# Performance work log

Measured on AMD Instinct MI355X. Metric: run time of the kernel, lower is better.

## Reference

```python
import jax, jax.numpy as jnp
import numpy as np

RRELU_SLOPE = (1.0 / 8.0 + 1.0 / 3.0) / 2.0  # F.rrelu eval-mode slope
DILATIONS = (1, 2, 4, 8)
HIDDEN_TEMP = 1.0
GUMBEL_TEMP = 0.1


def rrelu(x):
    return jnp.where(x >= 0, x, RRELU_SLOPE * x)


def conv1d(x, w, b, dilation):
    # x: [B, Cin, T], w: [Cout, Cin, K] -> [B, Cout, T'] (VALID, dilated)
    y = jax.lax.conv_general_dilated(
        x, w, window_strides=(1,), padding='VALID', rhs_dilation=(dilation,),
        dimension_numbers=('NCH', 'OIH', 'NCH'))
    return y + b[None, :, None]


def setup_inputs() -> dict:
    key = jax.random.key(0)
    ks = jax.random.split(key, 16)
    B, D, T, R = 8, 32, 4096, 8
    s = 0.05  # param scale for numerical stability
    inp = {
        'x': jax.random.normal(ks[0], (B, D, T), jnp.float32),
        'u': jax.random.uniform(ks[1], (B, T, R), jnp.float32, 1e-6, 1.0 - 1e-6),
        'conv_w0': jax.random.normal(ks[2], (128, D, 2), jnp.float32) * s,
        'conv_b0': jax.random.normal(ks[3], (128,), jnp.float32) * s,
        'conv_w1': jax.random.normal(ks[4], (128, 128, 2), jnp.float32) * s,
        'conv_b1': jax.random.normal(ks[5], (128,), jnp.float32) * s,
        'conv_w2': jax.random.normal(ks[6], (128, 128, 2), jnp.float32) * s,
        'conv_b2': jax.random.normal(ks[7], (128,), jnp.float32) * s,
        'conv_w3': jax.random.normal(ks[8], (R, 128, 2), jnp.float32) * s,
        'conv_b3': jax.random.normal(ks[9], (R,), jnp.float32) * s,
        'pw0': jax.random.normal(ks[10], (R, 256, 128), jnp.float32) * s,
        'pb0': jax.random.normal(ks[11], (R, 256), jnp.float32) * s,
        'pw1': jax.random.normal(ks[12], (R, 2 * D, 256), jnp.float32) * s,
        'pb1': jax.random.normal(ks[13], (R, 2 * D), jnp.float32) * s,
    }
    return inp


def reference(x, u, conv_w0, conv_b0, conv_w1, conv_b1, conv_w2, conv_b2,
              conv_w3, conv_b3, pw0, pb0, pw1, pb1):
    pad = sum(DILATIONS)  # causal left pad
    h = jnp.pad(x, ((0, 0), (0, 0), (pad, 0)))
    for w, b, d in ((conv_w0, conv_b0, DILATIONS[0]),
                    (conv_w1, conv_b1, DILATIONS[1]),
                    (conv_w2, conv_b2, DILATIONS[2])):
        h = rrelu(conv1d(h, w, b, d))
    pre = h  # [B, 128, T + dilations[-1]]
    h_vecs = rrelu(conv1d(pre, conv_w3, conv_b3, DILATIONS[3]))  # [B, R, T]
    pre = pre[:, :, DILATIONS[3]:]  # [B, 128, T]

    p = jax.nn.softmax(h_vecs / HIDDEN_TEMP, axis=1)  # [B, R, T]
    logits = jnp.log(p).transpose(0, 2, 1)  # [B, T, R]
    g = -jnp.log(-jnp.log(u))  # gumbel noise from uniform input
    gen_z = jax.nn.softmax((logits + g) / GUMBEL_TEMP, axis=-1).transpose(0, 2, 1)  # [B, R, T]

    # Fused mixture-of-experts dynamic linear: equal to materializing
    # einsum('brt,roi->boit') then contracting with pre, but avoids the huge tensor.
    params = (jnp.einsum('brt,roi,bit->bot', gen_z, pw0, pre)
              + jnp.einsum('brt,ro->bot', gen_z, pb0))
    # NOTE: original calls F.rrelu(params) without assignment -> no-op (kept faithful)
    params = (jnp.einsum('brt,roi,bit->bot', gen_z, pw1, params)
              + jnp.einsum('brt,ro->bot', gen_z, pb1))

    mus, sig = jnp.split(params, 2, axis=1)  # each [B, n_dims, T]
    sigmas = 0.5 + 0.5 * jnp.tanh(sig) + 0.001
    return mus, sigmas, gen_z
```

## Files before the change

### kernel.cpp

```cpp
#include <hip/hip_runtime.h>
#include <math.h>

typedef __attribute__((ext_vector_type(8))) short bf16x8;
typedef __attribute__((ext_vector_type(4))) float f32x4;
struct __align__(8)  us4 { unsigned short x,y,z,w; };
struct __align__(16) ui4 { unsigned x,y,z,w; };

#define SLOPE 0.2291666666666667f
constexpr int N0=4110, N1=4108, N2=4104, NX=4111;

__device__ __forceinline__ unsigned short f2bf(float f){
  unsigned u = __float_as_uint(f);
  u = (u + 0x7FFF + ((u>>16)&1)) >> 16;
  return (unsigned short)u;
}
__device__ __forceinline__ float bf2f(unsigned short h){
  return __uint_as_float(((unsigned)h)<<16);
}
__device__ __forceinline__ float rrelu(float v){ return v>=0.f ? v : v*SLOPE; }

__global__ __launch_bounds__(256) void prep_w(
  const float* __restrict__ w0, const float* __restrict__ w1, const float* __restrict__ w2,
  const float* __restrict__ pw0, const float* __restrict__ pw1,
  const float* __restrict__ pb0, const float* __restrict__ pb1,
  unsigned short* __restrict__ w0e, unsigned short* __restrict__ w1e, unsigned short* __restrict__ w2e,
  unsigned short* __restrict__ pw0b, unsigned short* __restrict__ pw1b,
  unsigned short* __restrict__ pb0e, unsigned short* __restrict__ pb1e)
{
  int idx = blockIdx.x*256 + threadIdx.x;
  if (idx < 8192){ int oc=idx>>6, k=idx&63, tap=k>>5, i=k&31;
    w0e[idx] = f2bf(w0[(oc*32+i)*2+tap]); return; }
  idx -= 8192;
  if (idx < 32768){ int oc=idx>>8, k=idx&255, tap=k>>7, i=k&127;
    w1e[idx] = f2bf(w1[(oc*128+i)*2+tap]); return; }
  idx -= 32768;
  if (idx < 32768){ int oc=idx>>8, k=idx&255, tap=k>>7, i=k&127;
    w2e[idx] = f2bf(w2[(oc*128+i)*2+tap]); return; }
  idx -= 32768;
  if (idx < 262144){ pw0b[idx] = f2bf(pw0[idx]); return; }
  idx -= 262144;
  if (idx < 131072){ pw1b[idx] = f2bf(pw1[idx]); return; }
  idx -= 131072;
  if (idx < 8192){ int o=idx>>5, r=idx&31; pb0e[idx] = r<8 ? f2bf(pb0[r*256+o]) : (unsigned short)0; return; }
  idx -= 8192;
  if (idx < 2048){ int o=idx>>5, r=idx&31; pb1e[idx] = r<8 ? f2bf(pb1[r*64+o]) : (unsigned short)0; return; }
}

__global__ __launch_bounds__(64) void prep_xt(const float* __restrict__ x,
                                              unsigned short* __restrict__ xt)
{
  __shared__ float s[32][64];
  const int b = blockIdx.y, j0 = blockIdx.x*64, l = threadIdx.x;
  #pragma unroll 4
  for (int i=0;i<32;i++){
    int p = j0 + l - 15;
    s[i][l] = (p>=0 && p<4096) ? x[((size_t)b*32+i)*4096+p] : 0.f;
  }
  __syncthreads();
  const int j = j0 + l;
  if (j < NX){
    unsigned tmp[16];
    #pragma unroll
    for (int q=0;q<16;q++)
      tmp[q] = (unsigned)f2bf(s[2*q][l]) | ((unsigned)f2bf(s[2*q+1][l])<<16);
    ui4* dst = (ui4*)(xt + ((size_t)b*NX + j)*32);
    #pragma unroll
    for (int q=0;q<4;q++){ ui4 v={tmp[4*q],tmp[4*q+1],tmp[4*q+2],tmp[4*q+3]}; dst[q]=v; }
  }
}

template<int IC, int DIL, int NIN, int NOUT>
__global__ __launch_bounds__(256) void conv_g(
    const unsigned short* __restrict__ act,
    const unsigned short* __restrict__ wgt,
    const float* __restrict__ bias,
    unsigned short* __restrict__ outp)
{
  constexpr int KT   = 2*IC;
  constexpr int NK   = KT/32;
  constexpr int NH   = (KT > 128) ? 2 : 1;
  constexpr int KPH  = KT / NH;
  constexpr int NKH  = KPH/32;
  constexpr int HRB  = KPH*2;
  constexpr int HCPR = HRB/16;
  __shared__ __align__(16) char wsm[64*HRB];
  __shared__ __align__(16) char outs[64*128];

  const int tid = threadIdx.x;
  const int b = blockIdx.z, ob = blockIdx.y, tb = blockIdx.x*64;
  const int o0g = ob*64;
  const int wid = tid>>6, l = tid&63, lo = l&15, hi = l>>4;

  bf16x8 bfr[NK];
  {
    const int tg = tb + wid*16 + lo;
    const int te = tg < NOUT ? tg : NOUT-1;
    #pragma unroll
    for (int kk=0;kk<NK;kk++){
      int k = kk*32 + hi*8;
      int tap = (k >= IC) ? 1 : 0;
      int off = k - tap*IC;
      bfr[kk] = *(const bf16x8*)(act + ((size_t)b*NIN + te + tap*DIL)*IC + off);
    }
  }

  f32x4 acc[4];
  #pragma unroll
  for (int m=0;m<4;m++) acc[m] = (f32x4){0.f,0.f,0.f,0.f};

  #pragma unroll
  for (int h=0; h<NH; ++h){
    __syncthreads();
    for (int c = tid; c < 64*HCPR; c += 256){
      int row = c / HCPR, cc = c % HCPR;
      ui4 v = *(const ui4*)((const char*)wgt + (size_t)(o0g+row)*KT*2 + h*HRB + cc*16);
      *(ui4*)(wsm + row*HRB + ((cc*16) ^ ((row&7)<<4))) = v;
    }
    __syncthreads();
    #pragma unroll
    for (int kk=0;kk<NKH;kk++){
      #pragma unroll
      for (int m=0;m<4;m++){
        int row = m*16 + lo;
        bf16x8 af = *(const bf16x8*)(wsm + row*HRB + ((kk*64+hi*16) ^ ((row&7)<<4)));
        acc[m] = __builtin_amdgcn_mfma_f32_16x16x32_bf16(af, bfr[h*NKH+kk], acc[m], 0,0,0);
      }
    }
  }
  __syncthreads();
  #pragma unroll
  for (int m=0;m<4;m++){
    const int ol = m*16 + hi*4;
    float b0v = bias[o0g+ol+0], b1v = bias[o0g+ol+1], b2v = bias[o0g+ol+2], b3v = bias[o0g+ol+3];
    int tl = wid*16 + lo;
    us4 v;
    v.x = f2bf(rrelu(acc[m][0] + b0v));
    v.y = f2bf(rrelu(acc[m][1] + b1v));
    v.z = f2bf(rrelu(acc[m][2] + b2v));
    v.w = f2bf(rrelu(acc[m][3] + b3v));
    *(us4*)(outs + tl*128 + ((ol*2) ^ ((tl&7)<<4))) = v;
  }
  __syncthreads();
  #pragma unroll
  for (int i=0;i<2;i++){
    int c = tid + i*256;
    int row = c>>3, cc = c&7;
    if (tb + row < NOUT){
      ui4 v = *(const ui4*)(outs + row*128 + ((cc*16) ^ ((row&7)<<4)));
      *(ui4*)(outp + ((size_t)b*NOUT + tb + row)*128 + o0g + cc*8) = v;
    }
  }
}

__global__ __launch_bounds__(64) void gumbel_g(
  const unsigned short* __restrict__ h2t,
  const float* __restrict__ w3, const float* __restrict__ b3,
  const float* __restrict__ u,
  float* __restrict__ genz,
  unsigned short* __restrict__ zt)
{
  __shared__ unsigned hs[72][66];
  const int b = blockIdx.y, t0 = blockIdx.x*64, l = threadIdx.x;
  const unsigned* src = (const unsigned*)(h2t + ((size_t)b*N2 + t0)*128);
  for (int e=l; e<72*64; e+=64) hs[e>>6][e&63] = src[e];
  __syncthreads();

  float acc[8];
  #pragma unroll
  for (int r=0;r<8;r++) acc[r]=b3[r];
  for (int i2=0;i2<64;i2++){
    unsigned a0 = hs[l][i2], a1 = hs[l+8][i2];
    float v00 = bf2f(a0&0xffff), v01 = bf2f(a0>>16);
    float v10 = bf2f(a1&0xffff), v11 = bf2f(a1>>16);
    const int i = 2*i2;
    #pragma unroll
    for (int r=0;r<8;r++){
      acc[r] = fmaf(w3[(r*128+i)*2],     v00, acc[r]);
      acc[r] = fmaf(w3[(r*128+i)*2+1],   v10, acc[r]);
      acc[r] = fmaf(w3[(r*128+i+1)*2],   v01, acc[r]);
      acc[r] = fmaf(w3[(r*128+i+1)*2+1], v11, acc[r]);
    }
  }
  float m = -1e30f;
  #pragma unroll
  for (int r=0;r<8;r++){ acc[r] = rrelu(acc[r]); m = fmaxf(m, acc[r]); }
  float s = 0.f;
  #pragma unroll
  for (int r=0;r<8;r++) s += __expf(acc[r]-m);
  const float lse = m + __logf(s);
  const int t = t0 + l;
  const float* ub = u + ((size_t)b*4096 + t)*8;
  float y[8], m2 = -1e30f;
  #pragma unroll
  for (int r=0;r<8;r++){
    float g = -__logf(-__logf(ub[r]));
    y[r] = (acc[r] - lse + g)*10.f;
    m2 = fmaxf(m2, y[r]);
  }
  float s2 = 0.f;
  #pragma unroll
  for (int r=0;r<8;r++){ y[r] = __expf(y[r]-m2); s2 += y[r]; }
  const float inv = 1.f/s2;
  #pragma unroll
  for (int r=0;r<8;r++){
    y[r] *= inv;
    genz[((size_t)b*8+r)*4096 + t] = y[r];
  }
  ui4 zp = { (unsigned)f2bf(y[0]) | ((unsigned)f2bf(y[1])<<16),
             (unsigned)f2bf(y[2]) | ((unsigned)f2bf(y[3])<<16),
             (unsigned)f2bf(y[4]) | ((unsigned)f2bf(y[5])<<16),
             (unsigned)f2bf(y[6]) | ((unsigned)f2bf(y[7])<<16) };
  ui4 zz = {0,0,0,0};
  ui4* zd = (ui4*)(zt + ((size_t)b*4096 + t)*32);
  zd[0]=zp; zd[1]=zz; zd[2]=zz; zd[3]=zz;
}

__global__ __launch_bounds__(256) void moe1_m(
  const unsigned short* __restrict__ h2t,
  const float* __restrict__ genz,
  const unsigned short* __restrict__ zt,
  const unsigned short* __restrict__ pw0b,
  const unsigned short* __restrict__ pb0e,
  unsigned short* __restrict__ hidt)
{
  __shared__ __align__(16) char pres[16384];
  __shared__ __align__(16) char outb[8192];
  __shared__ float zl[512];

  const int ob = blockIdx.x, b = blockIdx.z, tb = blockIdx.y*64;
  const int o0g = ob*64;
  const int tid = threadIdx.x;
  #pragma unroll
  for (int i=0;i<2;i++){
    int e = tid + i*256;
    zl[e] = genz[((size_t)b*8 + (e>>6))*4096 + tb + (e&63)];
  }
  {
    const char* src = (const char*)(h2t + ((size_t)b*N2 + tb + 8)*128);
    #pragma unroll
    for (int i=0;i<4;i++){
      int c = tid + i*256, row = c>>4, cc = c&15;
      ui4 v = *(const ui4*)(src + row*256 + cc*16);
      *(ui4*)(pres + row*256 + ((cc*16) ^ ((row&7)<<4))) = v;
    }
  }
  __syncthreads();

  const int wid = tid>>6, l = tid&63, lo = l&15, hi = l>>4;
  const int ow = o0g + wid*16;

  bf16x8 bfr[4][4];
  #pragma unroll
  for (int n=0;n<4;n++){
    int tl = n*16 + lo;
    #pragma unroll
    for (int kk=0;kk<4;kk++)
      bfr[n][kk] = *(const bf16x8*)(pres + tl*256 + ((kk*64 + hi*16) ^ ((tl&7)<<4)));
  }
  f32x4 acc[4];
  {
    bf16x8 pf = *(const bf16x8*)(pb0e + (size_t)(ow + lo)*32 + hi*8);
    #pragma unroll
    for (int n=0;n<4;n++){
      bf16x8 zf = *(const bf16x8*)(zt + ((size_t)b*4096 + tb + n*16 + lo)*32 + hi*8);
      acc[n] = __builtin_amdgcn_mfma_f32_16x16x32_bf16(pf, zf, (f32x4){0.f,0.f,0.f,0.f}, 0,0,0);
    }
  }

  const unsigned short* abase = pw0b + (size_t)(ow + lo)*128 + hi*8;
  bf16x8 A0[4], A1[4];
  #pragma unroll
  for (int kk=0;kk<4;kk++) A0[kk] = *(const bf16x8*)(abase + kk*32);
  #pragma unroll
  for (int kk=0;kk<4;kk++) A1[kk] = *(const bf16x8*)(abase + 32768 + kk*32);

  #pragma unroll
  for (int r=0;r<8;r++){
    f32x4 ar[4];
    #pragma unroll
    for (int n=0;n<4;n++) ar[n] = (f32x4){0.f,0.f,0.f,0.f};
    if ((r&1)==0){
      #pragma unroll
      for (int kk=0;kk<4;kk++)
        #pragma unroll
        for (int n=0;n<4;n++)
          ar[n] = __builtin_amdgcn_mfma_f32_16x16x32_bf16(A0[kk], bfr[n][kk], ar[n], 0,0,0);
      if (r < 6){
        #pragma unroll
        for (int kk=0;kk<4;kk++)
          A0[kk] = *(const bf16x8*)(abase + (size_t)(r+2)*32768 + kk*32);
      }
    } else {
      #pragma unroll
      for (int kk=0;kk<4;kk++)
        #pragma unroll
        for (int n=0;n<4;n++)
          ar[n] = __builtin_amdgcn_mfma_f32_16x16x32_bf16(A1[kk], bfr[n][kk], ar[n], 0,0,0);
      if (r < 6){
        #pragma unroll
        for (int kk=0;kk<4;kk++)
          A1[kk] = *(const bf16x8*)(abase + (size_t)(r+2)*32768 + kk*32);
      }
    }
    #pragma unroll
    for (int n=0;n<4;n++){
      float zv = zl[r*64 + n*16 + lo];
      #pragma unroll
      for (int c2=0;c2<4;c2++)
        acc[n][c2] = fmaf(zv, ar[n][c2], acc[n][c2]);
    }
  }

  #pragma unroll
  for (int n=0;n<4;n++){
    int tl = n*16 + lo;
    int ol2 = (wid*16 + hi*4)*2;
    us4 v;
    v.x=f2bf(acc[n][0]); v.y=f2bf(acc[n][1]); v.z=f2bf(acc[n][2]); v.w=f2bf(acc[n][3]);
    *(us4*)(outb + tl*128 + (ol2 ^ ((tl&7)<<4))) = v;
  }
  __syncthreads();
  #pragma unroll
  for (int i=0;i<2;i++){
    int c = tid + i*256, row = c>>3, cc = c&7;
    ui4 v = *(const ui4*)(outb + row*128 + ((cc*16) ^ ((row&7)<<4)));
    *(ui4*)(hidt + (((size_t)b*4 + ob)*4096 + tb + row)*64 + cc*8) = v;
  }
}

__global__ __launch_bounds__(256) void moe2_m(
  const unsigned short* __restrict__ hidt,
  const float* __restrict__ genz,
  const unsigned short* __restrict__ zt,
  const unsigned short* __restrict__ pw1b,
  const unsigned short* __restrict__ pb1e,
  float* __restrict__ out)
{
  __shared__ __align__(16) char hids[32768];
  __shared__ float zl[512];

  const int b = blockIdx.y, tb = blockIdx.x*64;
  const int tid = threadIdx.x;
  #pragma unroll
  for (int i=0;i<2;i++){
    int e = tid + i*256;
    zl[e] = genz[((size_t)b*8 + (e>>6))*4096 + tb + (e&63)];
  }
  #pragma unroll
  for (int i=0;i<8;i++){
    int c = tid + i*256, row = c>>5, cc = c&31;
    int obq = cc>>3, wi = cc&7;
    ui4 v = *(const ui4*)(hidt + (((size_t)b*4 + obq)*4096 + tb + row)*64 + wi*8);
    *(ui4*)(hids + row*512 + ((cc*16) ^ ((row&7)<<4))) = v;
  }
  __syncthreads();

  const int wid = tid>>6, l = tid&63, lo = l&15, hi = l>>4;
  const int ow = wid*16;

  f32x4 acc[4];
  {
    bf16x8 pf = *(const bf16x8*)(pb1e + (size_t)(ow + lo)*32 + hi*8);
    #pragma unroll
    for (int n=0;n<4;n++){
      bf16x8 zf = *(const bf16x8*)(zt + ((size_t)b*4096 + tb + n*16 + lo)*32 + hi*8);
      acc[n] = __builtin_amdgcn_mfma_f32_16x16x32_bf16(pf, zf, (f32x4){0.f,0.f,0.f,0.f}, 0,0,0);
    }
  }

  const unsigned short* abase = pw1b + (size_t)(ow + lo)*256 + hi*8;
  bf16x8 A0[8], A1[8];
  #pragma unroll
  for (int kk=0;kk<8;kk++) A0[kk] = *(const bf16x8*)(abase + kk*32);
  #pragma unroll
  for (int kk=0;kk<8;kk++) A1[kk] = *(const bf16x8*)(abase + 16384 + kk*32);

  #pragma unroll
  for (int r=0;r<8;r++){
    f32x4 ar[4];
    #pragma unroll
    for (int n=0;n<4;n++) ar[n] = (f32x4){0.f,0.f,0.f,0.f};
    if ((r&1)==0){
      #pragma unroll
      for (int kk=0;kk<8;kk++){
        #pragma unroll
        for (int n=0;n<4;n++){
          int tl = n*16 + lo;
          bf16x8 bf = *(const bf16x8*)(hids + tl*512 + ((kk*64 + hi*16) ^ ((tl&7)<<4)));
          ar[n] = __builtin_amdgcn_mfma_f32_16x16x32_bf16(A0[kk], bf, ar[n], 0,0,0);
        }
      }
      if (r < 6){
        #pragma unroll
        for (int kk=0;kk<8;kk++)
          A0[kk] = *(const bf16x8*)(abase + (size_t)(r+2)*16384 + kk*32);
      }
    } else {
      #pragma unroll
      for (int kk=0;kk<8;kk++){
        #pragma unroll
        for (int n=0;n<4;n++){
          int tl = n*16 + lo;
          bf16x8 bf = *(const bf16x8*)(hids + tl*512 + ((kk*64 + hi*16) ^ ((tl&7)<<4)));
          ar[n] = __builtin_amdgcn_mfma_f32_16x16x32_bf16(A1[kk], bf, ar[n], 0,0,0);
        }
      }
      if (r < 6){
        #pragma unroll
        for (int kk=0;kk<8;kk++)
          A1[kk] = *(const bf16x8*)(abase + (size_t)(r+2)*16384 + kk*32);
      }
    }
    #pragma unroll
    for (int n=0;n<4;n++){
      float zv = zl[r*64 + n*16 + lo];
      #pragma unroll
      for (int c2=0;c2<4;c2++)
        acc[n][c2] = fmaf(zv, ar[n][c2], acc[n][c2]);
    }
  }

  #pragma unroll
  for (int n=0;n<4;n++){
    int t = tb + n*16 + lo;
    #pragma unroll
    for (int c2=0;c2<4;c2++){
      int o = ow + hi*4 + c2;
      float v = acc[n][c2];
      if (o < 32)
        out[((size_t)b*32 + o)*4096 + t] = v;
      else {
        float e = __expf(2.f*v);
        float th = 1.f - 2.f/(e+1.f);
        out[(size_t)1048576 + ((size_t)b*32 + (o-32))*4096 + t] = 0.5f + 0.5f*th + 0.001f;
      }
    }
  }
}

extern "C" void kernel_launch(void* const* d_in, const int* in_sizes, int n_in,
                              void* d_out, int out_size, void* d_ws, size_t ws_size,
                              hipStream_t stream) {
  const float* x   = (const float*)d_in[0];
  const float* u   = (const float*)d_in[1];
  const float* w0  = (const float*)d_in[2];
  const float* b0  = (const float*)d_in[3];
  const float* w1  = (const float*)d_in[4];
  const float* b1  = (const float*)d_in[5];
  const float* w2  = (const float*)d_in[6];
  const float* b2  = (const float*)d_in[7];
  const float* w3  = (const float*)d_in[8];
  const float* b3  = (const float*)d_in[9];
  const float* pw0 = (const float*)d_in[10];
  const float* pb0 = (const float*)d_in[11];
  const float* pw1 = (const float*)d_in[12];
  const float* pb1 = (const float*)d_in[13];

  float* out  = (float*)d_out;
  float* genz = out + (size_t)2*8*32*4096;

  char* p = (char*)d_ws;
  unsigned short* xt   = (unsigned short*)p; p += 2104832;
  unsigned short* h0t  = (unsigned short*)p; p += 8417280;
  unsigned short* h1t  = (unsigned short*)p; p += 8413184;
  unsigned short* h2t  = (unsigned short*)p; p += 8404992;
  unsigned short* ztb  = (unsigned short*)p; p += 2097152;
  unsigned short* hidt = (unsigned short*)p; p += 16777216;
  unsigned short* w0e  = (unsigned short*)p; p += 16384;
  unsigned short* w1e  = (unsigned short*)p; p += 65536;
  unsigned short* w2e  = (unsigned short*)p; p += 65536;
  unsigned short* pw0b = (unsigned short*)p; p += 524288;
  unsigned short* pw1b = (unsigned short*)p; p += 262144;
  unsigned short* pb0e = (unsigned short*)p; p += 16384;
  unsigned short* pb1e = (unsigned short*)p; p += 4096;

  prep_w<<<1864, 256, 0, stream>>>(w0,w1,w2,pw0,pw1,pb0,pb1,
                                   w0e,w1e,w2e,pw0b,pw1b,pb0e,pb1e);
  prep_xt<<<dim3(65,8), 64, 0, stream>>>(x, xt);
  conv_g<32,1,NX,N0><<<dim3(65,2,8), 256, 0, stream>>>(xt,  w0e, b0, h0t);
  conv_g<128,2,N0,N1><<<dim3(65,2,8), 256, 0, stream>>>(h0t, w1e, b1, h1t);
  conv_g<128,4,N1,N2><<<dim3(65,2,8), 256, 0, stream>>>(h1t, w2e, b2, h2t);
  gumbel_g<<<dim3(64,8), 64, 0, stream>>>(h2t, w3, b3, u, genz, ztb);
  moe1_m<<<dim3(4,64,8), 256, 0, stream>>>(h2t, genz, ztb, pw0b, pb0e, hidt);
  moe2_m<<<dim3(64,8), 256, 0, stream>>>(hidt, genz, ztb, pw1b, pb1e, out);
}
```

Measured before the change: 136.9 us.

## Fuse the two MoE dynamic-linear kernels into one block-resident kernel

Merges moe1 and moe2 into a single 512-thread kernel. The 256-wide hidden activation for a 64-timestep tile now stays in shared memory instead of making a 16 MB bf16 round trip through global memory. The second stage splits K across wave pairs and reduces the halves through shared memory. In exchange, grid parallelism drops from 2048 blocks to 512, each block now reads the full pw0 set, and the A-fragment double-buffered register prefetch is replaced by inline loads.

```diff
diff --git a/kernel.cpp b/kernel.cpp
--- a/kernel.cpp
+++ b/kernel.cpp
@@ -215,224 +215,170 @@
   zd[0]=zp; zd[1]=zz; zd[2]=zz; zd[3]=zz;
 }
 
-__global__ __launch_bounds__(256) void moe1_m(
+__global__ __launch_bounds__(512) void moe_f(
   const unsigned short* __restrict__ h2t,
   const float* __restrict__ genz,
   const unsigned short* __restrict__ zt,
   const unsigned short* __restrict__ pw0b,
   const unsigned short* __restrict__ pb0e,
-  unsigned short* __restrict__ hidt)
-{
-  __shared__ __align__(16) char pres[16384];
-  __shared__ __align__(16) char outb[8192];
-  __shared__ float zl[512];
-
-  const int ob = blockIdx.x, b = blockIdx.z, tb = blockIdx.y*64;
-  const int o0g = ob*64;
-  const int tid = threadIdx.x;
-  #pragma unroll
-  for (int i=0;i<2;i++){
-    int e = tid + i*256;
-    zl[e] = genz[((size_t)b*8 + (e>>6))*4096 + tb + (e&63)];
-  }
-  {
-    const char* src = (const char*)(h2t + ((size_t)b*N2 + tb + 8)*128);
-    #pragma unroll
-    for (int i=0;i<4;i++){
-      int c = tid + i*256, row = c>>4, cc = c&15;
-      ui4 v = *(const ui4*)(src + row*256 + cc*16);
-      *(ui4*)(pres + row*256 + ((cc*16) ^ ((row&7)<<4))) = v;
-    }
-  }
-  __syncthreads();
-
-  const int wid = tid>>6, l = tid&63, lo = l&15, hi = l>>4;
-  const int ow = o0g + wid*16;
-
-  bf16x8 bfr[4][4];
-  #pragma unroll
-  for (int n=0;n<4;n++){
-    int tl = n*16 + lo;
-    #pragma unroll
-    for (int kk=0;kk<4;kk++)
-      bfr[n][kk] = *(const bf16x8*)(pres + tl*256 + ((kk*64 + hi*16) ^ ((tl&7)<<4)));
-  }
-  f32x4 acc[4];
-  {
-    bf16x8 pf = *(const bf16x8*)(pb0e + (size_t)(ow + lo)*32 + hi*8);
-    #pragma unroll
-    for (int n=0;n<4;n++){
-      bf16x8 zf = *(const bf16x8*)(zt + ((size_t)b*4096 + tb + n*16 + lo)*32 + hi*8);
-      acc[n] = __builtin_amdgcn_mfma_f32_16x16x32_bf16(pf, zf, (f32x4){0.f,0.f,0.f,0.f}, 0,0,0);
-    }
-  }
-
-  const unsigned short* abase = pw0b + (size_t)(ow + lo)*128 + hi*8;
-  bf16x8 A0[4], A1[4];
-  #pragma unroll
-  for (int kk=0;kk<4;kk++) A0[kk] = *(const bf16x8*)(abase + kk*32);
-  #pragma unroll
-  for (int kk=0;kk<4;kk++) A1[kk] = *(const bf16x8*)(abase + 32768 + kk*32);
-
-  #pragma unroll
-  for (int r=0;r<8;r++){
-    f32x4 ar[4];
-    #pragma unroll
-    for (int n=0;n<4;n++) ar[n] = (f32x4){0.f,0.f,0.f,0.f};
-    if ((r&1)==0){
-      #pragma unroll
-      for (int kk=0;kk<4;kk++)
-        #pragma unroll
-        for (int n=0;n<4;n++)
-          ar[n] = __builtin_amdgcn_mfma_f32_16x16x32_bf16(A0[kk], bfr[n][kk], ar[n], 0,0,0);
-      if (r < 6){
-        #pragma unroll
-        for (int kk=0;kk<4;kk++)
-          A0[kk] = *(const bf16x8*)(abase + (size_t)(r+2)*32768 + kk*32);
-      }
-    } else {
-      #pragma unroll
-      for (int kk=0;kk<4;kk++)
-        #pragma unroll
-        for (int n=0;n<4;n++)
-          ar[n] = __builtin_amdgcn_mfma_f32_16x16x32_bf16(A1[kk], bfr[n][kk], ar[n], 0,0,0);
-      if (r < 6){
-        #pragma unroll
-        for (int kk=0;kk<4;kk++)
-          A1[kk] = *(const bf16x8*)(abase + (size_t)(r+2)*32768 + kk*32);
-      }
-    }
-    #pragma unroll
-    for (int n=0;n<4;n++){
-      float zv = zl[r*64 + n*16 + lo];
-      #pragma unroll
-      for (int c2=0;c2<4;c2++)
-        acc[n][c2] = fmaf(zv, ar[n][c2], acc[n][c2]);
-    }
-  }
-
-  #pragma unroll
-  for (int n=0;n<4;n++){
-    int tl = n*16 + lo;
-    int ol2 = (wid*16 + hi*4)*2;
-    us4 v;
-    v.x=f2bf(acc[n][0]); v.y=f2bf(acc[n][1]); v.z=f2bf(acc[n][2]); v.w=f2bf(acc[n][3]);
-    *(us4*)(outb + tl*128 + (ol2 ^ ((tl&7)<<4))) = v;
-  }
-  __syncthreads();
-  #pragma unroll
-  for (int i=0;i<2;i++){
-    int c = tid + i*256, row = c>>3, cc = c&7;
-    ui4 v = *(const ui4*)(outb + row*128 + ((cc*16) ^ ((row&7)<<4)));
-    *(ui4*)(hidt + (((size_t)b*4 + ob)*4096 + tb + row)*64 + cc*8) = v;
-  }
-}
-
-__global__ __launch_bounds__(256) void moe2_m(
-  const unsigned short* __restrict__ hidt,
-  const float* __restrict__ genz,
-  const unsigned short* __restrict__ zt,
   const unsigned short* __restrict__ pw1b,
   const unsigned short* __restrict__ pb1e,
   float* __restrict__ out)
 {
+  __shared__ __align__(16) char pres[16384];
   __shared__ __align__(16) char hids[32768];
   __shared__ float zl[512];
 
   const int b = blockIdx.y, tb = blockIdx.x*64;
   const int tid = threadIdx.x;
-  #pragma unroll
-  for (int i=0;i<2;i++){
-    int e = tid + i*256;
-    zl[e] = genz[((size_t)b*8 + (e>>6))*4096 + tb + (e&63)];
-  }
-  #pragma unroll
-  for (int i=0;i<8;i++){
-    int c = tid + i*256, row = c>>5, cc = c&31;
-    int obq = cc>>3, wi = cc&7;
-    ui4 v = *(const ui4*)(hidt + (((size_t)b*4 + obq)*4096 + tb + row)*64 + wi*8);
-    *(ui4*)(hids + row*512 + ((cc*16) ^ ((row&7)<<4))) = v;
+  zl[tid] = genz[((size_t)b*8 + (tid>>6))*4096 + tb + (tid&63)];
+  {
+    const char* src = (const char*)(h2t + ((size_t)b*N2 + tb + 8)*128);
+    #pragma unroll
+    for (int i=0;i<2;i++){
+      int c = tid + i*512, row = c>>4, cc = c&15;
+      ui4 v = *(const ui4*)(src + row*256 + cc*16);
+      *(ui4*)(pres + row*256 + ((cc*16) ^ ((row&7)<<4))) = v;
+    }
   }
   __syncthreads();
 
   const int wid = tid>>6, l = tid&63, lo = l&15, hi = l>>4;
-  const int ow = wid*16;
-
-  f32x4 acc[4];
-  {
-    bf16x8 pf = *(const bf16x8*)(pb1e + (size_t)(ow + lo)*32 + hi*8);
-    #pragma unroll
-    for (int n=0;n<4;n++){
-      bf16x8 zf = *(const bf16x8*)(zt + ((size_t)b*4096 + tb + n*16 + lo)*32 + hi*8);
-      acc[n] = __builtin_amdgcn_mfma_f32_16x16x32_bf16(pf, zf, (f32x4){0.f,0.f,0.f,0.f}, 0,0,0);
-    }
-  }
-
-  const unsigned short* abase = pw1b + (size_t)(ow + lo)*256 + hi*8;
-  bf16x8 A0[8], A1[8];
-  #pragma unroll
-  for (int kk=0;kk<8;kk++) A0[kk] = *(const bf16x8*)(abase + kk*32);
-  #pragma unroll
-  for (int kk=0;kk<8;kk++) A1[kk] = *(const bf16x8*)(abase + 16384 + kk*32);
-
+
+  const int ow = wid*32;
+  bf16x8 bfr[4][4];
+  #pragma unroll
+  for (int n=0;n<4;n++){
+    int tl = n*16 + lo;
+    #pragma unroll
+    for (int kk=0;kk<4;kk++)
+      bfr[n][kk] = *(const bf16x8*)(pres + tl*256 + ((kk*64 + hi*16) ^ ((tl&7)<<4)));
+  }
+  bf16x8 zfr[4];
+  #pragma unroll
+  for (int n=0;n<4;n++)
+    zfr[n] = *(const bf16x8*)(zt + ((size_t)b*4096 + tb + n*16 + lo)*32 + hi*8);
+
+  f32x4 acc[2][4];
+  #pragma unroll
+  for (int m=0;m<2;m++){
+    bf16x8 pf = *(const bf16x8*)(pb0e + (size_t)(ow + m*16 + lo)*32 + hi*8);
+    #pragma unroll
+    for (int n=0;n<4;n++)
+      acc[m][n] = __builtin_amdgcn_mfma_f32_16x16x32_bf16(pf, zfr[n], (f32x4){0.f,0.f,0.f,0.f}, 0,0,0);
+  }
+
+  const unsigned short* abase0 = pw0b + (size_t)(ow + lo)*128 + hi*8;
   #pragma unroll
   for (int r=0;r<8;r++){
-    f32x4 ar[4];
-    #pragma unroll
-    for (int n=0;n<4;n++) ar[n] = (f32x4){0.f,0.f,0.f,0.f};
-    if ((r&1)==0){
-      #pragma unroll
-      for (int kk=0;kk<8;kk++){
-        #pragma unroll
-        for (int n=0;n<4;n++){
-          int tl = n*16 + lo;
-          bf16x8 bf = *(const bf16x8*)(hids + tl*512 + ((kk*64 + hi*16) ^ ((tl&7)<<4)));
-          ar[n] = __builtin_amdgcn_mfma_f32_16x16x32_bf16(A0[kk], bf, ar[n], 0,0,0);
-        }
-      }
-      if (r < 6){
-        #pragma unroll
-        for (int kk=0;kk<8;kk++)
-          A0[kk] = *(const bf16x8*)(abase + (size_t)(r+2)*16384 + kk*32);
-      }
-    } else {
-      #pragma unroll
-      for (int kk=0;kk<8;kk++){
-        #pragma unroll
-        for (int n=0;n<4;n++){
-          int tl = n*16 + lo;
-          bf16x8 bf = *(const bf16x8*)(hids + tl*512 + ((kk*64 + hi*16) ^ ((tl&7)<<4)));
-          ar[n] = __builtin_amdgcn_mfma_f32_16x16x32_bf16(A1[kk], bf, ar[n], 0,0,0);
-        }
-      }
-      if (r < 6){
-        #pragma unroll
-        for (int kk=0;kk<8;kk++)
-          A1[kk] = *(const bf16x8*)(abase + (size_t)(r+2)*16384 + kk*32);
+    f32x4 ar[2][4];
+    #pragma unroll
+    for (int m=0;m<2;m++)
+      #pragma unroll
+      for (int n=0;n<4;n++) ar[m][n] = (f32x4){0.f,0.f,0.f,0.f};
+    #pragma unroll
+    for (int kk=0;kk<4;kk++){
+      bf16x8 A0 = *(const bf16x8*)(abase0 + (size_t)r*32768 + kk*32);
+      bf16x8 A1 = *(const bf16x8*)(abase0 + (size_t)r*32768 + 2048 + kk*32);
+      #pragma unroll
+      for (int n=0;n<4;n++){
+        ar[0][n] = __builtin_amdgcn_mfma_f32_16x16x32_bf16(A0, bfr[n][kk], ar[0][n], 0,0,0);
+        ar[1][n] = __builtin_amdgcn_mfma_f32_16x16x32_bf16(A1, bfr[n][kk], ar[1][n], 0,0,0);
       }
     }
     #pragma unroll
     for (int n=0;n<4;n++){
       float zv = zl[r*64 + n*16 + lo];
       #pragma unroll
+      for (int m=0;m<2;m++)
+        #pragma unroll
+        for (int c2=0;c2<4;c2++)
+          acc[m][n][c2] = fmaf(zv, ar[m][n][c2], acc[m][n][c2]);
+    }
+  }
+
+  #pragma unroll
+  for (int m=0;m<2;m++){
+    int ol2 = (ow + m*16 + hi*4)*2;
+    #pragma unroll
+    for (int n=0;n<4;n++){
+      int tl = n*16 + lo;
+      us4 v;
+      v.x=f2bf(acc[m][n][0]); v.y=f2bf(acc[m][n][1]);
+      v.z=f2bf(acc[m][n][2]); v.w=f2bf(acc[m][n][3]);
+      *(us4*)(hids + tl*512 + (ol2 ^ ((tl&7)<<4))) = v;
+    }
+  }
+  __syncthreads();
+
+  const int kh = wid & 1, oq = wid >> 1;
+  const int ow2 = oq*16;
+
+  bf16x8 bfr2[4][4];
+  #pragma unroll
+  for (int n=0;n<4;n++){
+    int tl = n*16 + lo;
+    #pragma unroll
+    for (int kk=0;kk<4;kk++)
+      bfr2[n][kk] = *(const bf16x8*)(hids + tl*512 + ((kh*256 + kk*64 + hi*16) ^ ((tl&7)<<4)));
+  }
+  f32x4 acc2[4];
+  if (kh == 0){
+    bf16x8 pf = *(const bf16x8*)(pb1e + (size_t)(ow2 + lo)*32 + hi*8);
+    #pragma unroll
+    for (int n=0;n<4;n++)
+      acc2[n] = __builtin_amdgcn_mfma_f32_16x16x32_bf16(pf, zfr[n], (f32x4){0.f,0.f,0.f,0.f}, 0,0,0);
+  } else {
+    #pragma unroll
+    for (int n=0;n<4;n++) acc2[n] = (f32x4){0.f,0.f,0.f,0.f};
+  }
+
+  const unsigned short* abase1 = pw1b + (size_t)(ow2 + lo)*256 + kh*128 + hi*8;
+  #pragma unroll
+  for (int r=0;r<8;r++){
+    f32x4 ar2[4];
+    #pragma unroll
+    for (int n=0;n<4;n++) ar2[n] = (f32x4){0.f,0.f,0.f,0.f};
+    #pragma unroll
+    for (int kk=0;kk<4;kk++){
+      bf16x8 A2 = *(const bf16x8*)(abase1 + (size_t)r*16384 + kk*32);
+      #pragma unroll
+      for (int n=0;n<4;n++)
+        ar2[n] = __builtin_amdgcn_mfma_f32_16x16x32_bf16(A2, bfr2[n][kk], ar2[n], 0,0,0);
+    }
+    #pragma unroll
+    for (int n=0;n<4;n++){
+      float zv = zl[r*64 + n*16 + lo];
+      #pragma unroll
       for (int c2=0;c2<4;c2++)
-        acc[n][c2] = fmaf(zv, ar[n][c2], acc[n][c2]);
-    }
-  }
-
-  #pragma unroll
-  for (int n=0;n<4;n++){
-    int t = tb + n*16 + lo;
-    #pragma unroll
-    for (int c2=0;c2<4;c2++){
-      int o = ow + hi*4 + c2;
-      float v = acc[n][c2];
-      if (o < 32)
-        out[((size_t)b*32 + o)*4096 + t] = v;
-      else {
-        float e = __expf(2.f*v);
-        float th = 1.f - 2.f/(e+1.f);
-        out[(size_t)1048576 + ((size_t)b*32 + (o-32))*4096 + t] = 0.5f + 0.5f*th + 0.001f;
+        acc2[n][c2] = fmaf(zv, ar2[n][c2], acc2[n][c2]);
+    }
+  }
+
+  float* red = (float*)pres;
+  if (kh == 1){
+    #pragma unroll
+    for (int n=0;n<4;n++)
+      #pragma unroll
+      for (int c2=0;c2<4;c2++)
+        red[(ow2 + hi*4 + c2)*64 + n*16 + lo] = acc2[n][c2];
+  }
+  __syncthreads();
+  if (kh == 0){
+    #pragma unroll
+    for (int n=0;n<4;n++){
+      int t = tb + n*16 + lo;
+      #pragma unroll
+      for (int c2=0;c2<4;c2++){
+        int o = ow2 + hi*4 + c2;
+        float v = acc2[n][c2] + red[o*64 + n*16 + lo];
+        if (o < 32)
+          out[((size_t)b*32 + o)*4096 + t] = v;
+        else {
+          float e = __expf(2.f*v);
+          float th = 1.f - 2.f/(e+1.f);
+          out[(size_t)1048576 + ((size_t)b*32 + (o-32))*4096 + t] = 0.5f + 0.5f*th + 0.001f;
+        }
       }
     }
   }
@@ -465,7 +411,6 @@
   unsigned short* h1t  = (unsigned short*)p; p += 8413184;
   unsigned short* h2t  = (unsigned short*)p; p += 8404992;
   unsigned short* ztb  = (unsigned short*)p; p += 2097152;
-  unsigned short* hidt = (unsigned short*)p; p += 16777216;
   unsigned short* w0e  = (unsigned short*)p; p += 16384;
   unsigned short* w1e  = (unsigned short*)p; p += 65536;
   unsigned short* w2e  = (unsigned short*)p; p += 65536;
@@ -481,6 +426,5 @@
   conv_g<128,2,N0,N1><<<dim3(65,2,8), 256, 0, stream>>>(h0t, w1e, b1, h1t);
   conv_g<128,4,N1,N2><<<dim3(65,2,8), 256, 0, stream>>>(h1t, w2e, b2, h2t);
   gumbel_g<<<dim3(64,8), 64, 0, stream>>>(h2t, w3, b3, u, genz, ztb);
-  moe1_m<<<dim3(4,64,8), 256, 0, stream>>>(h2t, genz, ztb, pw0b, pb0e, hidt);
-  moe2_m<<<dim3(64,8), 256, 0, stream>>>(hidt, genz, ztb, pw1b, pb1e, out);
-}
+  moe_f<<<dim3(64,8), 512, 0, stream>>>(h2t, genz, ztb, pw0b, pb0e, pw1b, pb1e, out);
+}
```

Measured after the change: 161.7 us. 1.18x slower.
